# Kernel tuning notes

Measured on AMD Instinct MI355X. Metric: run time of the kernel, lower is better.

## Reference

```python
import jax, jax.numpy as jnp
import numpy as np

NUM_FIELDS = 32  # m
EMBED = 64       # d
HIDDEN = 256     # conv output channels per layer


def setup_inputs() -> dict:
    key = jax.random.key(0)
    ks = jax.random.split(key, 8)
    m, d, H = NUM_FIELDS, EMBED, HIDDEN
    prev = [m, H // 2, H // 2]  # prev_dim entering each layer (split_half)
    x = jax.random.normal(ks[0], (1024, m, d), dtype=jnp.float32)
    W0 = jax.random.normal(ks[1], (m * prev[0], H), dtype=jnp.float32) * 0.02
    W1 = jax.random.normal(ks[2], (m * prev[1], H), dtype=jnp.float32) * 0.02
    W2 = jax.random.normal(ks[3], (m * prev[2], H), dtype=jnp.float32) * 0.02
    b0 = jnp.zeros((H,), jnp.float32)
    b1 = jnp.zeros((H,), jnp.float32)
    b2 = jnp.zeros((H,), jnp.float32)
    fc_in = H // 2 + H // 2 + H  # 512
    fc_W = jax.random.normal(ks[4], (fc_in, 1), dtype=jnp.float32) * 0.02
    fc_b = jnp.zeros((1,), jnp.float32)
    return {"x": x, "W0": W0, "b0": b0, "W1": W1, "b1": b1,
            "W2": W2, "b2": b2, "fc_W": fc_W, "fc_b": fc_b}


def _cin_forward(x, Ws, bs, fc_W, fc_b):
    num_layers = len(Ws)
    x0 = x  # (b, m, d)
    h = x
    xs = []
    for i in range(num_layers):
        b_, m, d = x0.shape
        n = h.shape[1]
        # outer product interaction: (b, m, n, d) -> flatten field pairs
        z = jnp.einsum('bmd,bnd->bmnd', x0, h).reshape(b_, m * n, d)
        # 1x1 Conv1D over channel dim (m*n): (b, k, d),(k, H) -> (b, H, d)
        y = jax.nn.relu(jnp.einsum('bkd,kh->bhd', z, Ws[i]) + bs[i][None, :, None])
        if i != num_layers - 1:  # split_half
            half = y.shape[1] // 2
            xcur, h = y[:, :half], y[:, half:]
        else:
            xcur = y
            h = y
        xs.append(xcur)
    f = jnp.concatenate(xs, axis=1)  # (b, fc_in, d)
    f = jnp.sum(f, axis=2)           # (b, fc_in)
    return f @ fc_W + fc_b           # (b, 1)


def reference(x, W0, b0, W1, b1, W2, b2, fc_W, fc_b):
    return _cin_forward(x, [W0, W1, W2], [b0, b1, b2], fc_W, fc_b)
```

## Files before the change

### kernel.cpp

```cpp
#include <hip/hip_runtime.h>

typedef __attribute__((ext_vector_type(8))) short bf16x8;
typedef __attribute__((ext_vector_type(4))) float f32x4;

__device__ __forceinline__ float bf2f(unsigned short u){
    unsigned int v = ((unsigned int)u) << 16;
    return __builtin_bit_cast(float, v);
}
__device__ __forceinline__ unsigned short f2bf(float f){
    unsigned int u = __builtin_bit_cast(unsigned int, f);
    u += 0x7FFFu + ((u >> 16) & 1u);
    return (unsigned short)(u >> 16);
}
__device__ __forceinline__ unsigned int cvt_pk_bf16(float lo, float hi){
    unsigned int r;
    asm("v_cvt_pk_bf16_f32 %0, %1, %2" : "=v"(r) : "v"(lo), "v"(hi));
    return r;
}
__device__ __forceinline__ unsigned int mulpack(unsigned int u, float xf){
    float flo = __builtin_bit_cast(float, u << 16);
    float fhi = __builtin_bit_cast(float, u & 0xffff0000u);
    return cvt_pk_bf16(xf * flo, xf * fhi);
}

__global__ void prep_wt(const float* __restrict__ W, unsigned short* __restrict__ Wt, int K){
    __shared__ float tile[64][65];
    const int k0 = blockIdx.x * 64;
    const int j0 = blockIdx.y * 64;
    const int t  = threadIdx.x;
    #pragma unroll
    for (int it = 0; it < 16; it++){
        int idx = it * 256 + t;
        int kr = idx >> 6, jc = idx & 63;
        tile[kr][jc] = W[(size_t)(k0 + kr) * 256 + j0 + jc];
    }
    __syncthreads();
    #pragma unroll
    for (int it = 0; it < 2; it++){
        int idx = it * 256 + t;
        int jr = idx >> 3, kc = (idx & 7) << 3;
        uint4 tv;
        unsigned short* ts = (unsigned short*)&tv;
        #pragma unroll
        for (int q = 0; q < 8; q++)
            ts[q] = f2bf(tile[kc + q][jr]);
        *(uint4*)(Wt + (size_t)(j0 + jr) * K + k0 + kc) = tv;
    }
}

__global__ void prep_x(const float* __restrict__ x, unsigned short* __restrict__ Xt){
    int b = blockIdx.x;
    int t = threadIdx.x;
    #pragma unroll
    for (int it = 0; it < 8; it++){
        int o = it * 256 + t;
        int d = o >> 5, m = o & 31;
        Xt[(size_t)b * 2048 + o] = f2bf(x[(size_t)b * 2048 + m * 64 + d]);
    }
}

__global__ void init_out(float* __restrict__ out, const float* __restrict__ fcb){
    int i = blockIdx.x * 256 + threadIdx.x;
    if (i < 1024) out[i] = fcb[0];
}

template<int NN, int LOG2NN, int KTOT, int JX, bool HAS_HOUT>
__global__ __launch_bounds__(256, 2) void cin_stage(
    const unsigned short* __restrict__ Xt,
    const unsigned short* __restrict__ Hin,
    const unsigned short* __restrict__ Wt,
    const float* __restrict__ bias,
    const float* __restrict__ fcW,
    unsigned short* __restrict__ Hout,
    float* __restrict__ out)
{
    constexpr int KT = KTOT / 32;
    constexpr int ZS = 40;
    constexpr int XS = 40;
    constexpr int HS = (NN == 32) ? XS : 136;

    __shared__ unsigned short smem[32768];
    unsigned short* const Zb0 = smem;
    unsigned short* const Zb1 = smem + 5120;
    unsigned short* const Xl  = smem + 10240;
    unsigned short* const Hl  = (NN == 32) ? Xl : (smem + 15360);
    unsigned short* const Yl  = smem + 15360;

    const int t    = threadIdx.x;
    const int lane = t & 63;
    const int w    = t >> 6;
    const int li   = lane & 15;
    const int lq   = lane >> 4;
    const int bpair = blockIdx.x;

    {
        const int c  = t >> 1;
        const int b  = bpair * 2 + (c >> 6);
        const int d  = c & 63;
        const int mh = (t & 1) << 4;
        const uint4* xsrc = (const uint4*)(Xt + ((size_t)b << 11) + (d << 5) + mh);
        uint4 x0 = xsrc[0], x1 = xsrc[1];
        *(uint4*)(Xl + c * XS + mh)     = x0;
        *(uint4*)(Xl + c * XS + mh + 8) = x1;
        if (NN == 128){
            const int nh = (t & 1) << 6;
            const uint4* hsrc = (const uint4*)(Hin + (size_t)((b << 6) + d) * 128 + nh);
            #pragma unroll
            for (int q = 0; q < 8; q++){
                uint4 hv = hsrc[q];
                *(uint4*)(Hl + c * HS + nh + q * 8) = hv;
            }
        }
    }
    __syncthreads();

    const int zc  = t & 127;
    const int zkh = t >> 7;
    auto build = [&](unsigned short* zbuf, int kt){
        const int kg = (kt << 5) + (zkh << 4);
        const int m  = kg >> LOG2NN;
        const int n0 = kg & (NN - 1);
        float xf = bf2f(Xl[zc * XS + m]);
        const uint4* hsrc = (const uint4*)(Hl + zc * HS + n0);
        uint4 h0 = hsrc[0], h1 = hsrc[1];
        uint4 z0, z1;
        z0.x = mulpack(h0.x, xf);
        z0.y = mulpack(h0.y, xf);
        z0.z = mulpack(h0.z, xf);
        z0.w = mulpack(h0.w, xf);
        z1.x = mulpack(h1.x, xf);
        z1.y = mulpack(h1.y, xf);
        z1.z = mulpack(h1.z, xf);
        z1.w = mulpack(h1.w, xf);
        uint4* zdst = (uint4*)(zbuf + zc * ZS + (zkh << 4));
        zdst[0] = z0;
        zdst[1] = z1;
    };

    const unsigned short* wbase = Wt + (size_t)((w << 6) + li) * KTOT + (lq << 3);
    auto loadA = [&](int kt, bf16x8* A){
        const unsigned short* wk = wbase + (kt << 5);
        #pragma unroll
        for (int jt = 0; jt < 4; jt++)
            A[jt] = *(const bf16x8*)(wk + (size_t)jt * 16 * KTOT);
    };

    f32x4 acc[4][8];
    #pragma unroll
    for (int jt = 0; jt < 4; jt++)
        #pragma unroll
        for (int ct = 0; ct < 8; ct++)
            acc[jt][ct] = (f32x4){0.f, 0.f, 0.f, 0.f};

    build(Zb0, 0);
    bf16x8 Acur[4];
    loadA(0, Acur);
    __syncthreads();

    for (int kt = 0; kt < KT; kt++){
        unsigned short* const Zr = (kt & 1) ? Zb1 : Zb0;
        unsigned short* const Zw = (kt & 1) ? Zb0 : Zb1;
        bf16x8 Anx[4];
        loadA(kt + 1 < KT ? kt + 1 : kt, Anx);
        #pragma unroll
        for (int ct = 0; ct < 8; ct++){
            bf16x8 B = *(const bf16x8*)(Zr + ((ct << 4) + li) * ZS + (lq << 3));
            #pragma unroll
            for (int jt = 0; jt < 4; jt++)
                acc[jt][ct] = __builtin_amdgcn_mfma_f32_16x16x32_bf16(Acur[jt], B, acc[jt][ct], 0, 0, 0);
        }
        if (kt + 1 < KT) build(Zw, kt + 1);
        #pragma unroll
        for (int jt = 0; jt < 4; jt++) Acur[jt] = Anx[jt];
        __syncthreads();
    }

    float pfc0 = 0.f, pfc1 = 0.f;
    #pragma unroll
    for (int jt = 0; jt < 4; jt++){
        const int jb = (w << 6) + (jt << 4) + (lq << 2);
        float bv[4], fv[4];
        #pragma unroll
        for (int r = 0; r < 4; r++){
            int j = jb + r;
            bv[r] = bias[j];
            fv[r] = (j < JX) ? fcW[j] : 0.f;
        }
        #pragma unroll
        for (int ct = 0; ct < 8; ct++){
            f32x4 f = acc[jt][ct];
            int c = (ct << 4) + li;
            float ps = 0.f;
            #pragma unroll
            for (int r = 0; r < 4; r++){
                float y = f[r] + bv[r];
                y = y > 0.f ? y : 0.f;
                ps += fv[r] * y;
                if (HAS_HOUT){
                    int j = jb + r;
                    if (j >= 128)
                        Yl[(j - 128) * 136 + c] = f2bf(y);
                }
            }
            if (ct < 4) pfc0 += ps; else pfc1 += ps;
        }
    }
    #pragma unroll
    for (int off = 32; off; off >>= 1){
        pfc0 += __shfl_xor(pfc0, off, 64);
        pfc1 += __shfl_xor(pfc1, off, 64);
    }
    if (lane == 0){
        atomicAdd(out + bpair * 2 + 0, pfc0);
        atomicAdd(out + bpair * 2 + 1, pfc1);
    }

    if (HAS_HOUT){
        __syncthreads();
        const int c  = t >> 1;
        const int nh = (t & 1) << 6;
        unsigned short* gdst = Hout + (size_t)(bpair * 128 + c) * 128 + nh;
        #pragma unroll
        for (int i8 = 0; i8 < 8; i8++){
            uint4 tv;
            unsigned short* tmp = (unsigned short*)&tv;
            #pragma unroll
            for (int q = 0; q < 8; q++)
                tmp[q] = Yl[(nh + i8 * 8 + q) * 136 + c];
            *(uint4*)(gdst + i8 * 8) = tv;
        }
    }
}

extern "C" void kernel_launch(void* const* d_in, const int* in_sizes, int n_in,
                              void* d_out, int out_size, void* d_ws, size_t ws_size,
                              hipStream_t stream){
    const float* x   = (const float*)d_in[0];
    const float* W0  = (const float*)d_in[1];
    const float* b0  = (const float*)d_in[2];
    const float* W1  = (const float*)d_in[3];
    const float* b1  = (const float*)d_in[4];
    const float* W2  = (const float*)d_in[5];
    const float* b2  = (const float*)d_in[6];
    const float* fcW = (const float*)d_in[7];
    const float* fcb = (const float*)d_in[8];
    float* out = (float*)d_out;

    char* ws = (char*)d_ws;
    unsigned short* Xt  = (unsigned short*)(ws);
    unsigned short* Wt0 = (unsigned short*)(ws + 4194304);
    unsigned short* Wt1 = (unsigned short*)(ws + 4718592);
    unsigned short* Wt2 = (unsigned short*)(ws + 6815744);
    unsigned short* H0  = (unsigned short*)(ws + 8912896);
    unsigned short* H1  = (unsigned short*)(ws + 25690112);

    prep_wt<<<dim3(16, 4), 256, 0, stream>>>(W0, Wt0, 1024);
    prep_wt<<<dim3(64, 4), 256, 0, stream>>>(W1, Wt1, 4096);
    prep_wt<<<dim3(64, 4), 256, 0, stream>>>(W2, Wt2, 4096);
    prep_x <<<1024, 256, 0, stream>>>(x, Xt);
    init_out<<<4, 256, 0, stream>>>(out, fcb);

    cin_stage< 32, 5, 1024, 128, true ><<<512, 256, 0, stream>>>(Xt, Xt, Wt0, b0, fcW,       H0, out);
    cin_stage<128, 7, 4096, 128, true ><<<512, 256, 0, stream>>>(Xt, H0, Wt1, b1, fcW + 128, H1, out);
    cin_stage<128, 7, 4096, 256, false><<<512, 256, 0, stream>>>(Xt, H1, Wt2, b2, fcW + 256, nullptr, out);
}
```

Before: 383.3 us.

## Double K-step per barrier with XOR-swizzled LDS layouts for Z and H

Each loop iteration now processes two 32-wide K slices, building a 64-wide Z tile so there are half as many __syncthreads barriers. X is stored transposed in LDS so each thread reads its scalar from a column. The H and Z buffers use XOR swizzles to cut LDS bank conflicts. The changes raise LDS footprint and index arithmetic, and may affect occupancy at two blocks per CU.

```diff
diff --git a/kernel.cpp b/kernel.cpp
--- a/kernel.cpp
+++ b/kernel.cpp
@@ -74,67 +74,88 @@
     unsigned short* __restrict__ Hout,
     float* __restrict__ out)
 {
-    constexpr int KT = KTOT / 32;
-    constexpr int ZS = 40;
-    constexpr int XS = 40;
-    constexpr int HS = (NN == 32) ? XS : 136;
-
-    __shared__ unsigned short smem[32768];
-    unsigned short* const Zb0 = smem;
-    unsigned short* const Zb1 = smem + 5120;
-    unsigned short* const Xl  = smem + 10240;
-    unsigned short* const Hl  = (NN == 32) ? Xl : (smem + 15360);
-    unsigned short* const Yl  = smem + 15360;
+    constexpr int KT  = KTOT / 32;
+    constexpr int KT2 = KTOT / 64;
+    constexpr int XTS = 136;
+    constexpr int HS  = (NN == 128) ? 136 : 40;
+    constexpr int HM  = (NN == 128) ? 7 : 3;
+    constexpr int ZSB = 72;
+    constexpr int XTSZ = 32 * XTS;
+    constexpr int HLSZ = 128 * HS;
+    constexpr int ZBSZ = 128 * ZSB;
+    constexpr int NEED = XTSZ + HLSZ + 2 * ZBSZ;
+    constexpr int SMSZ = NEED > 17408 ? NEED : 17408;
+
+    __shared__ unsigned short smem[SMSZ];
+    unsigned short* const Xlt = smem;
+    unsigned short* const Hl  = smem + XTSZ;
+    unsigned short* const Zb0 = smem + XTSZ + HLSZ;
+    unsigned short* const Zb1 = Zb0 + ZBSZ;
+    unsigned short* const Yl  = smem;
 
     const int t    = threadIdx.x;
     const int lane = t & 63;
     const int w    = t >> 6;
     const int li   = lane & 15;
     const int lq   = lane >> 4;
+    const int lh   = li >> 3;
     const int bpair = blockIdx.x;
 
     {
         const int c  = t >> 1;
         const int b  = bpair * 2 + (c >> 6);
         const int d  = c & 63;
-        const int mh = (t & 1) << 4;
+        const int half = t & 1;
+        const int mh = half << 4;
         const uint4* xsrc = (const uint4*)(Xt + ((size_t)b << 11) + (d << 5) + mh);
         uint4 x0 = xsrc[0], x1 = xsrc[1];
-        *(uint4*)(Xl + c * XS + mh)     = x0;
-        *(uint4*)(Xl + c * XS + mh + 8) = x1;
+        const unsigned short* xs0 = (const unsigned short*)&x0;
+        const unsigned short* xs1 = (const unsigned short*)&x1;
+        #pragma unroll
+        for (int q = 0; q < 8; q++) Xlt[(mh + q) * XTS + c]     = xs0[q];
+        #pragma unroll
+        for (int q = 0; q < 8; q++) Xlt[(mh + 8 + q) * XTS + c] = xs1[q];
         if (NN == 128){
-            const int nh = (t & 1) << 6;
-            const uint4* hsrc = (const uint4*)(Hin + (size_t)((b << 6) + d) * 128 + nh);
+            const uint4* hsrc = (const uint4*)(Hin + (size_t)((b << 6) + d) * 128 + (half << 6));
             #pragma unroll
             for (int q = 0; q < 8; q++){
                 uint4 hv = hsrc[q];
-                *(uint4*)(Hl + c * HS + nh + q * 8) = hv;
+                const int sub = ((half << 3) + q) ^ ((c >> 3) & 7);
+                *(uint4*)(Hl + c * HS + (sub << 3)) = hv;
             }
+        } else {
+            const int s0 = ((half << 1) + 0) ^ ((c >> 3) & 3);
+            const int s1 = ((half << 1) + 1) ^ ((c >> 3) & 3);
+            *(uint4*)(Hl + c * HS + (s0 << 3)) = x0;
+            *(uint4*)(Hl + c * HS + (s1 << 3)) = x1;
         }
     }
     __syncthreads();
 
     const int zc  = t & 127;
     const int zkh = t >> 7;
-    auto build = [&](unsigned short* zbuf, int kt){
-        const int kg = (kt << 5) + (zkh << 4);
-        const int m  = kg >> LOG2NN;
-        const int n0 = kg & (NN - 1);
-        float xf = bf2f(Xl[zc * XS + m]);
-        const uint4* hsrc = (const uint4*)(Hl + zc * HS + n0);
-        uint4 h0 = hsrc[0], h1 = hsrc[1];
-        uint4 z0, z1;
-        z0.x = mulpack(h0.x, xf);
-        z0.y = mulpack(h0.y, xf);
-        z0.z = mulpack(h0.z, xf);
-        z0.w = mulpack(h0.w, xf);
-        z1.x = mulpack(h1.x, xf);
-        z1.y = mulpack(h1.y, xf);
-        z1.z = mulpack(h1.z, xf);
-        z1.w = mulpack(h1.w, xf);
-        uint4* zdst = (uint4*)(zbuf + zc * ZS + (zkh << 4));
-        zdst[0] = z0;
-        zdst[1] = z1;
+    const int zq  = (zc >> 3) & 7;
+    auto build = [&](unsigned short* zbuf, int ktp){
+        #pragma unroll
+        for (int qi = 0; qi < 2; qi++){
+            const int qq = (zkh << 1) + qi;
+            const int kg = (ktp << 6) + (qq << 4);
+            const int m  = kg >> LOG2NN;
+            const int n0 = kg & (NN - 1);
+            const float xf = bf2f(Xlt[m * XTS + zc]);
+            #pragma unroll
+            for (int j = 0; j < 2; j++){
+                const int hsub = ((n0 >> 3) + j) ^ (zq & HM);
+                uint4 hv = *(const uint4*)(Hl + zc * HS + (hsub << 3));
+                uint4 zv;
+                zv.x = mulpack(hv.x, xf);
+                zv.y = mulpack(hv.y, xf);
+                zv.z = mulpack(hv.z, xf);
+                zv.w = mulpack(hv.w, xf);
+                const int zsub = ((qq << 1) + j) ^ zq;
+                *(uint4*)(zbuf + zc * ZSB + (zsub << 3)) = zv;
+            }
+        }
     };
 
     const unsigned short* wbase = Wt + (size_t)((w << 6) + li) * KTOT + (lq << 3);
@@ -153,25 +174,35 @@
             acc[jt][ct] = (f32x4){0.f, 0.f, 0.f, 0.f};
 
     build(Zb0, 0);
-    bf16x8 Acur[4];
-    loadA(0, Acur);
+    bf16x8 A0[4], A1[4];
+    loadA(0, A0);
     __syncthreads();
 
-    for (int kt = 0; kt < KT; kt++){
-        unsigned short* const Zr = (kt & 1) ? Zb1 : Zb0;
-        unsigned short* const Zw = (kt & 1) ? Zb0 : Zb1;
-        bf16x8 Anx[4];
-        loadA(kt + 1 < KT ? kt + 1 : kt, Anx);
+    for (int ktp = 0; ktp < KT2; ktp++){
+        unsigned short* const Zr = (ktp & 1) ? Zb1 : Zb0;
+        unsigned short* const Zw = (ktp & 1) ? Zb0 : Zb1;
+        const int kt0 = ktp << 1;
+        loadA(kt0 + 1, A1);
         #pragma unroll
         for (int ct = 0; ct < 8; ct++){
-            bf16x8 B = *(const bf16x8*)(Zr + ((ct << 4) + li) * ZS + (lq << 3));
+            const int row = (ct << 4) + li;
+            const int sub = lq ^ (((ct << 1) + lh) & 7);
+            bf16x8 B = *(const bf16x8*)(Zr + row * ZSB + (sub << 3));
             #pragma unroll
             for (int jt = 0; jt < 4; jt++)
-                acc[jt][ct] = __builtin_amdgcn_mfma_f32_16x16x32_bf16(Acur[jt], B, acc[jt][ct], 0, 0, 0);
-        }
-        if (kt + 1 < KT) build(Zw, kt + 1);
-        #pragma unroll
-        for (int jt = 0; jt < 4; jt++) Acur[jt] = Anx[jt];
+                acc[jt][ct] = __builtin_amdgcn_mfma_f32_16x16x32_bf16(A0[jt], B, acc[jt][ct], 0, 0, 0);
+        }
+        loadA(kt0 + 2 < KT ? kt0 + 2 : KT - 1, A0);
+        #pragma unroll
+        for (int ct = 0; ct < 8; ct++){
+            const int row = (ct << 4) + li;
+            const int sub = (4 + lq) ^ (((ct << 1) + lh) & 7);
+            bf16x8 B = *(const bf16x8*)(Zr + row * ZSB + (sub << 3));
+            #pragma unroll
+            for (int jt = 0; jt < 4; jt++)
+                acc[jt][ct] = __builtin_amdgcn_mfma_f32_16x16x32_bf16(A1[jt], B, acc[jt][ct], 0, 0, 0);
+        }
+        if (ktp + 1 < KT2) build(Zw, ktp + 1);
         __syncthreads();
     }
 
```

Result: no change. 384.1 us (+0.2%).
